# Kernel tuning notes

Hardware: AMD Instinct MI355X
Metric: run time of the kernel (lower is better)

## Reference

```python
import jax, jax.numpy as jnp
from jax import lax
import numpy as np

SEQ, BATCH, IN, HID = 1024, 8192, 3, 50


def setup_inputs() -> dict:
    key = jax.random.key(0)
    ks = jax.random.split(key, 7)
    s_ih = 1.0 / np.sqrt(HID)
    return {
        "x": jax.random.normal(ks[0], (SEQ, BATCH, IN), dtype=jnp.float32),
        "W_ih": jax.random.normal(ks[1], (4 * HID, IN), dtype=jnp.float32) * s_ih,
        "W_hh": jax.random.normal(ks[2], (4 * HID, HID), dtype=jnp.float32) * s_ih,
        "b_ih": jax.random.normal(ks[3], (4 * HID,), dtype=jnp.float32) * s_ih,
        "b_hh": jax.random.normal(ks[4], (4 * HID,), dtype=jnp.float32) * s_ih,
        "fc_w": jax.random.normal(ks[5], (1, HID), dtype=jnp.float32) * s_ih,
        "fc_b": jax.random.normal(ks[6], (1,), dtype=jnp.float32) * s_ih,
    }


def reference(x, W_ih, W_hh, b_ih, b_hh, fc_w, fc_b):
    # x: (T, B, I); PyTorch LSTM gate order is i, f, g, o along the 4H axis.
    T, B, _ = x.shape
    H = W_hh.shape[1]
    # Hoist the input projection out of the recurrence: one big GEMM.
    xg = jnp.einsum("tbi,gi->tbg", x, W_ih) + b_ih + b_hh  # (T, B, 4H)

    def step(carry, xg_t):
        h, c = carry
        gates = xg_t + h @ W_hh.T  # (B, 4H)
        i, f, g, o = jnp.split(gates, 4, axis=-1)
        i = jax.nn.sigmoid(i)
        f = jax.nn.sigmoid(f)
        g = jnp.tanh(g)
        o = jax.nn.sigmoid(o)
        c = f * c + i * g
        h = o * jnp.tanh(c)
        return (h, c), None

    h0 = jnp.zeros((B, H), dtype=x.dtype)
    c0 = jnp.zeros((B, H), dtype=x.dtype)
    (h_last, _), _ = lax.scan(step, (h0, c0), xg)
    # h.squeeze(0) in the torch code -> last layer's final hidden state (B, H)
    return h_last @ fc_w.T + fc_b  # (B, 1)
```

## Files before the change

kernel.cpp:

```cpp
#include <hip/hip_runtime.h>

#define SEQ   1024
#define BATCH 8192
#define HID   50
#define BT    32
#define CHS   16
#define NCH   (SEQ/CHS)
#define CHF   (CHS*BT*3)

typedef _Float16 half8 __attribute__((ext_vector_type(8)));
typedef float    f32x4 __attribute__((ext_vector_type(4)));

__device__ __forceinline__ int bslot(int k, int b){
  return (k >> 5)*512 + ((k & 31) >> 3)*128 + b*8 + (k & 7);
}

#define MFMA16(A,B,C) __builtin_amdgcn_mfma_f32_16x16x32_f16(A,B,C,0,0,0)

#define XLD(cg) {                                                          \
    const int f1 = tid + 512, f2 = tid + 1024;                             \
    const int s0_ = (tid*683) >> 16, s1_ = (f1*683) >> 16,                 \
              s2_ = (f2*683) >> 16;                                        \
    xr0 = x[(size_t)(((cg)*CHS + s0_)*BATCH + b0)*3 + (tid - 96*s0_)];     \
    xr1 = x[(size_t)(((cg)*CHS + s1_)*BATCH + b0)*3 + (f1  - 96*s1_)];     \
    xr2 = x[(size_t)(((cg)*CHS + s2_)*BATCH + b0)*3 + (f2  - 96*s2_)]; }

#define ELEM(acc, C, bq, slot) {                                              \
    const float Ei = __builtin_amdgcn_exp2f((acc)[0]);                        \
    const float Ef = __builtin_amdgcn_exp2f((acc)[1]);                        \
    const float Eg = __builtin_amdgcn_exp2f(fminf((acc)[2], 60.0f));          \
    const float Eo = __builtin_amdgcn_exp2f((acc)[3]);                        \
    const float di = 1.0f + Ei, df = 1.0f + Ef, dg = 1.0f + Eg;               \
    const float digg = di*dg;                                                 \
    const float r1 = __builtin_amdgcn_rcpf(digg*df);                          \
    const float t2 = __builtin_fmaf(Eg, 2.88539008177792f,                    \
                                    -2.88539008177792f);                      \
    const float num = __builtin_fmaf(C, digg, t2*df);                         \
    C = num*r1;                                                               \
    const float Ec = __builtin_amdgcn_exp2f(fminf(C, 80.0f));                 \
    const float r2 = __builtin_amdgcn_rcpf((1.0f+Eo)*(1.0f+Ec));              \
    (bq)[slot] = (_Float16)((Ec - 1.0f)*r2); }

__global__ __launch_bounds__(512, 2)
void lstm_g3(const float* __restrict__ x,
             const float* __restrict__ W_ih,
             const float* __restrict__ W_hh,
             const float* __restrict__ b_ih,
             const float* __restrict__ b_hh,
             const float* __restrict__ fc_w,
             const float* __restrict__ fc_b,
             float* __restrict__ out)
{
  __shared__ _Float16 Bst[2][2][1024];
  __shared__ float    xb[2][CHF];

  const int tid  = threadIdx.x;
  const int w    = tid >> 6;
  const int lane = tid & 63;
  const int r16  = lane & 15;
  const int grp  = lane >> 4;
  const int b0   = blockIdx.x * BT;
  const float L2E = 1.44269504088896f;

  const int  t1    = w;
  const int  t2    = (w < 5) ? (8 + w) : (5 + w);
  const bool hasA2 = (w < 5);
  const bool hasB2 = (w < 2) || (w >= 5);

  half8 Af[2][2];
  #pragma unroll
  for (int it = 0; it < 2; ++it) {
    const int tile = it ? t2 : t1;
    #pragma unroll
    for (int kh = 0; kh < 2; ++kh) {
      half8 f;
      #pragma unroll
      for (int i = 0; i < 8; ++i) {
        const int k = kh*32 + grp*8 + i;
        const int c = tile*16 + r16;
        float wv = 0.0f;
        if (c < 4*HID) {
          const int j = c >> 2, gi = c & 3;
          const int go = gi*HID + j;
          const float sc = (gi == 2) ? (2.0f*L2E) : (-L2E);
          if (k < HID)      wv = W_hh[go*HID + k] * sc;
          else if (k < 53)  wv = W_ih[go*3 + (k-50)] * sc;
          else if (k == 53) wv = (b_ih[go] + b_hh[go]) * sc;
        }
        f[i] = (_Float16)wv;
      }
      Af[it][kh] = f;
    }
  }

  const int j2  = t2*4 + grp;
  const int ws1 = bslot(t1*4 + grp, r16);
  const int ws2 = bslot((j2 < HID) ? j2 : 0, r16);
  const bool m2 = (j2 < HID);

  #pragma unroll
  for (int i = 0; i < 4; ++i) ((unsigned*)Bst)[tid + 512*i] = 0u;
  __syncthreads();
  if (tid < 64) Bst[tid >> 5][(tid >> 4) & 1][768 + (tid & 15)*8 + 5] = (_Float16)1.0f;

  float xr0, xr1, xr2;
  XLD(0); xb[0][tid] = xr0; xb[0][tid+512] = xr1; xb[0][tid+1024] = xr2;
  XLD(1); xb[1][tid] = xr0; xb[1][tid+512] = xr1; xb[1][tid+1024] = xr2;
  XLD(2);
  __syncthreads();
  if (tid < 96) {
    const int g = tid >= 48, l = tid - 48*g;
    const int bb = (l*171) >> 9, e = l - 3*bb;
    Bst[g][0][768 + bb*8 + 2 + e] = (_Float16)xb[0][tid];
  }
  __syncthreads();

  float csA0 = 0.f, csA1 = 0.f, csB0 = 0.f, csB1 = 0.f;

  auto step = [&](int t, int p, int q) {
    _Float16* bqA = &Bst[0][q][0];
    _Float16* bqB = &Bst[1][q][0];
    if ((w == 6 || w == 7) && lane < 48) {
      const int tn = t + 1;
      const int bb = (lane*171) >> 9, e = lane - 3*bb;
      const float xv = xb[(tn >> 4) & 1][(tn & 15)*96 + (w - 6)*48 + lane];
      (w == 6 ? bqA : bqB)[768 + bb*8 + 2 + e] = (_Float16)xv;
    }
    const half8 sA0 = *(const half8*)&Bst[0][p][lane*8];
    const half8 sA1 = *(const half8*)&Bst[0][p][512 + lane*8];
    const half8 sB0 = *(const half8*)&Bst[1][p][lane*8];
    const half8 sB1 = *(const half8*)&Bst[1][p][512 + lane*8];
    f32x4 aA0 = {0.f,0.f,0.f,0.f}, aB0 = {0.f,0.f,0.f,0.f};
    aA0 = MFMA16(Af[0][0], sA0, aA0);  aA0 = MFMA16(Af[0][1], sA1, aA0);
    aB0 = MFMA16(Af[0][0], sB0, aB0);  aB0 = MFMA16(Af[0][1], sB1, aB0);
    if (hasA2) {
      f32x4 aA1 = {0.f,0.f,0.f,0.f};
      aA1 = MFMA16(Af[1][0], sA0, aA1);  aA1 = MFMA16(Af[1][1], sA1, aA1);
      if (m2) ELEM(aA1, csA1, bqA, ws2);
    }
    if (hasB2) {
      f32x4 aB1 = {0.f,0.f,0.f,0.f};
      aB1 = MFMA16(Af[1][0], sB0, aB1);  aB1 = MFMA16(Af[1][1], sB1, aB1);
      if (m2) ELEM(aB1, csB1, bqB, ws2);
    }
    ELEM(aA0, csA0, bqA, ws1);
    ELEM(aB0, csB0, bqB, ws1);
    asm volatile("s_waitcnt lgkmcnt(0)\n\ts_barrier" ::: "memory");
  };

  #pragma unroll 1
  for (int tc = 0; tc < NCH; ++tc) {
    if (tc > 0) {
      const int pc = (tc + 1) & 1;
      xb[pc][tid] = xr0; xb[pc][tid+512] = xr1; xb[pc][tid+1024] = xr2;
      if (tc + 2 < NCH) { XLD(tc+2); }
    }
    const int tb = tc*CHS;
    #pragma unroll 1
    for (int u = 0; u < CHS/2; ++u) {
      step(tb + 2*u,     0, 1);
      step(tb + 2*u + 1, 1, 0);
    }
  }

  __syncthreads();
  if (tid < BT) {
    const int g = tid >> 4, b = tid & 15;
    float s = fc_b[0];
    #pragma unroll
    for (int j = 0; j < HID; ++j)
      s += fc_w[j] * (float)Bst[g][0][bslot(j, b)];
    out[b0 + tid] = s;
  }
}

extern "C" void kernel_launch(void* const* d_in, const int* in_sizes, int n_in,
                              void* d_out, int out_size, void* d_ws, size_t ws_size,
                              hipStream_t stream)
{
  const float* x    = (const float*)d_in[0];
  const float* W_ih = (const float*)d_in[1];
  const float* W_hh = (const float*)d_in[2];
  const float* b_ih = (const float*)d_in[3];
  const float* b_hh = (const float*)d_in[4];
  const float* fc_w = (const float*)d_in[5];
  const float* fc_b = (const float*)d_in[6];
  lstm_g3<<<BATCH/BT, 512, 65536, stream>>>(x, W_ih, W_hh, b_ih, b_hh,
                                            fc_w, fc_b, (float*)d_out);
}
```

Before: 555.6 us.

## Halve batch tile to 16 per block with 4 waves and inline x injection

```diff
diff --git a/kernel.cpp b/kernel.cpp
--- a/kernel.cpp
+++ b/kernel.cpp
@@ -3,10 +3,9 @@
 #define SEQ   1024
 #define BATCH 8192
 #define HID   50
-#define BT    32
+#define BT    16
 #define CHS   16
 #define NCH   (SEQ/CHS)
-#define CHF   (CHS*BT*3)
 
 typedef _Float16 half8 __attribute__((ext_vector_type(8)));
 typedef float    f32x4 __attribute__((ext_vector_type(4)));
@@ -18,12 +17,23 @@
 #define MFMA16(A,B,C) __builtin_amdgcn_mfma_f32_16x16x32_f16(A,B,C,0,0,0)
 
 #define XLD(cg) {                                                          \
-    const int f1 = tid + 512, f2 = tid + 1024;                             \
-    const int s0_ = (tid*683) >> 16, s1_ = (f1*683) >> 16,                 \
-              s2_ = (f2*683) >> 16;                                        \
-    xr0 = x[(size_t)(((cg)*CHS + s0_)*BATCH + b0)*3 + (tid - 96*s0_)];     \
-    xr1 = x[(size_t)(((cg)*CHS + s1_)*BATCH + b0)*3 + (f1  - 96*s1_)];     \
-    xr2 = x[(size_t)(((cg)*CHS + s2_)*BATCH + b0)*3 + (f2  - 96*s2_)]; }
+    const int f1 = tid + 256, f2 = tid + 512;                              \
+    const int s0_ = (tid*683) >> 15, s1_ = (f1*683) >> 15,                 \
+              s2_ = (f2*683) >> 15;                                        \
+    xr0 = x[(size_t)(((cg)*CHS + s0_)*BATCH + b0)*3 + (tid - 48*s0_)];     \
+    xr1 = x[(size_t)(((cg)*CHS + s1_)*BATCH + b0)*3 + (f1  - 48*s1_)];     \
+    xr2 = x[(size_t)(((cg)*CHS + s2_)*BATCH + b0)*3 + (f2  - 48*s2_)]; }
+
+#define XCOMMIT(bf) {                                                      \
+    const int f1 = tid + 256, f2 = tid + 512;                              \
+    const int s0_ = (tid*683) >> 15, s1_ = (f1*683) >> 15,                 \
+              s2_ = (f2*683) >> 15;                                        \
+    const int r0_ = tid - 48*s0_, r1_ = f1 - 48*s1_, r2_ = f2 - 48*s2_;    \
+    const int b0_ = (r0_*171) >> 9, b1_ = (r1_*171) >> 9,                  \
+              b2_ = (r2_*171) >> 9;                                        \
+    xs[bf][s0_][b0_][r0_ - 3*b0_] = (_Float16)xr0;                         \
+    xs[bf][s1_][b1_][r1_ - 3*b1_] = (_Float16)xr1;                         \
+    xs[bf][s2_][b2_][r2_ - 3*b2_] = (_Float16)xr2; }
 
 #define ELEM(acc, C, bq, slot) {                                              \
     const float Ei = __builtin_amdgcn_exp2f((acc)[0]);                        \
@@ -41,8 +51,8 @@
     const float r2 = __builtin_amdgcn_rcpf((1.0f+Eo)*(1.0f+Ec));              \
     (bq)[slot] = (_Float16)((Ec - 1.0f)*r2); }
 
-__global__ __launch_bounds__(512, 2)
-void lstm_g3(const float* __restrict__ x,
+__global__ __launch_bounds__(256, 2)
+void lstm_ph(const float* __restrict__ x,
              const float* __restrict__ W_ih,
              const float* __restrict__ W_hh,
              const float* __restrict__ b_ih,
@@ -51,8 +61,8 @@
              const float* __restrict__ fc_b,
              float* __restrict__ out)
 {
-  __shared__ _Float16 Bst[2][2][1024];
-  __shared__ float    xb[2][CHF];
+  __shared__ _Float16 Bst[2][1024];
+  __shared__ _Float16 xs[2][CHS][16][4];
 
   const int tid  = threadIdx.x;
   const int w    = tid >> 6;
@@ -62,15 +72,13 @@
   const int b0   = blockIdx.x * BT;
   const float L2E = 1.44269504088896f;
 
-  const int  t1    = w;
-  const int  t2    = (w < 5) ? (8 + w) : (5 + w);
-  const bool hasA2 = (w < 5);
-  const bool hasB2 = (w < 2) || (w >= 5);
+  const int  vw = (blockIdx.x & 1) ? (3 - w) : w;
+  const int  nt = (vw == 3) ? 4 : 3;
 
-  half8 Af[2][2];
+  half8 Af[4][2];
   #pragma unroll
-  for (int it = 0; it < 2; ++it) {
-    const int tile = it ? t2 : t1;
+  for (int it = 0; it < 4; ++it) {
+    const int tile = (it < 3) ? (vw + 4*it) : 12;
     #pragma unroll
     for (int kh = 0; kh < 2; ++kh) {
       half8 f;
@@ -93,83 +101,73 @@
     }
   }
 
-  const int j2  = t2*4 + grp;
-  const int ws1 = bslot(t1*4 + grp, r16);
-  const int ws2 = bslot((j2 < HID) ? j2 : 0, r16);
-  const bool m2 = (j2 < HID);
+  int wsl[4];
+  #pragma unroll
+  for (int it = 0; it < 4; ++it) {
+    const int tile = (it < 3) ? (vw + 4*it) : 12;
+    const int j = tile*4 + grp;
+    wsl[it] = bslot((j < HID) ? j : 0, r16);
+  }
 
   #pragma unroll
-  for (int i = 0; i < 4; ++i) ((unsigned*)Bst)[tid + 512*i] = 0u;
-  __syncthreads();
-  if (tid < 64) Bst[tid >> 5][(tid >> 4) & 1][768 + (tid & 15)*8 + 5] = (_Float16)1.0f;
+  for (int i = 0; i < 4; ++i) ((unsigned*)Bst)[tid + 256*i] = 0u;
+  #pragma unroll
+  for (int i2 = 0; i2 < 2; ++i2) {
+    const int i = tid + 256*i2;
+    xs[i >> 8][(i >> 4) & 15][i & 15][3] = (_Float16)1.0f;
+  }
 
   float xr0, xr1, xr2;
-  XLD(0); xb[0][tid] = xr0; xb[0][tid+512] = xr1; xb[0][tid+1024] = xr2;
-  XLD(1); xb[1][tid] = xr0; xb[1][tid+512] = xr1; xb[1][tid+1024] = xr2;
-  XLD(2);
-  __syncthreads();
-  if (tid < 96) {
-    const int g = tid >= 48, l = tid - 48*g;
-    const int bb = (l*171) >> 9, e = l - 3*bb;
-    Bst[g][0][768 + bb*8 + 2 + e] = (_Float16)xb[0][tid];
-  }
+  XLD(0);
+  XCOMMIT(0);
+  XLD(1);
   __syncthreads();
 
-  float csA0 = 0.f, csA1 = 0.f, csB0 = 0.f, csB1 = 0.f;
+  if (blockIdx.x & 1) __builtin_amdgcn_s_sleep(4);
 
-  auto step = [&](int t, int p, int q) {
-    _Float16* bqA = &Bst[0][q][0];
-    _Float16* bqB = &Bst[1][q][0];
-    if ((w == 6 || w == 7) && lane < 48) {
-      const int tn = t + 1;
-      const int bb = (lane*171) >> 9, e = lane - 3*bb;
-      const float xv = xb[(tn >> 4) & 1][(tn & 15)*96 + (w - 6)*48 + lane];
-      (w == 6 ? bqA : bqB)[768 + bb*8 + 2 + e] = (_Float16)xv;
+  float cs[4] = {0.f, 0.f, 0.f, 0.f};
+  const _Float16* xsp = &xs[0][0][0][0];
+
+  auto STEP = [&](int tsv, int p, int q) {
+    const half8 s0 = *(const half8*)&Bst[p][lane*8];
+    uint4 s1d = *(const uint4*)&Bst[p][512 + lane*8];
+    const uint2 xd = *(const uint2*)&xsp[tsv*64 + r16*4];
+    if (grp == 2) { s1d.y = xd.x; s1d.z = xd.y; }
+    const half8 s1 = __builtin_bit_cast(half8, s1d);
+    f32x4 a[4];
+    #pragma unroll
+    for (int it = 0; it < 4; ++it) if (it < nt) {
+      f32x4 z = {0.f, 0.f, 0.f, 0.f};
+      z = MFMA16(Af[it][0], s0, z);
+      a[it] = MFMA16(Af[it][1], s1, z);
     }
-    const half8 sA0 = *(const half8*)&Bst[0][p][lane*8];
-    const half8 sA1 = *(const half8*)&Bst[0][p][512 + lane*8];
-    const half8 sB0 = *(const half8*)&Bst[1][p][lane*8];
-    const half8 sB1 = *(const half8*)&Bst[1][p][512 + lane*8];
-    f32x4 aA0 = {0.f,0.f,0.f,0.f}, aB0 = {0.f,0.f,0.f,0.f};
-    aA0 = MFMA16(Af[0][0], sA0, aA0);  aA0 = MFMA16(Af[0][1], sA1, aA0);
-    aB0 = MFMA16(Af[0][0], sB0, aB0);  aB0 = MFMA16(Af[0][1], sB1, aB0);
-    if (hasA2) {
-      f32x4 aA1 = {0.f,0.f,0.f,0.f};
-      aA1 = MFMA16(Af[1][0], sA0, aA1);  aA1 = MFMA16(Af[1][1], sA1, aA1);
-      if (m2) ELEM(aA1, csA1, bqA, ws2);
-    }
-    if (hasB2) {
-      f32x4 aB1 = {0.f,0.f,0.f,0.f};
-      aB1 = MFMA16(Af[1][0], sB0, aB1);  aB1 = MFMA16(Af[1][1], sB1, aB1);
-      if (m2) ELEM(aB1, csB1, bqB, ws2);
-    }
-    ELEM(aA0, csA0, bqA, ws1);
-    ELEM(aB0, csB0, bqB, ws1);
+    _Float16* bq = &Bst[q][0];
+    #pragma unroll
+    for (int it = 0; it < 3; ++it) ELEM(a[it], cs[it], bq, wsl[it]);
+    if (nt == 4 && grp < 2) ELEM(a[3], cs[3], bq, wsl[3]);
     asm volatile("s_waitcnt lgkmcnt(0)\n\ts_barrier" ::: "memory");
   };
 
   #pragma unroll 1
   for (int tc = 0; tc < NCH; ++tc) {
-    if (tc > 0) {
-      const int pc = (tc + 1) & 1;
-      xb[pc][tid] = xr0; xb[pc][tid+512] = xr1; xb[pc][tid+1024] = xr2;
+    if (tc + 1 < NCH) {
+      XCOMMIT((tc + 1) & 1);
       if (tc + 2 < NCH) { XLD(tc+2); }
     }
-    const int tb = tc*CHS;
-    #pragma unroll 1
-    for (int u = 0; u < CHS/2; ++u) {
-      step(tb + 2*u,     0, 1);
-      step(tb + 2*u + 1, 1, 0);
+    xsp = &xs[tc & 1][0][0][0];
+    #pragma unroll 2
+    for (int ts = 0; ts < CHS; ts += 2) {
+      STEP(ts,     0, 1);
+      STEP(ts + 1, 1, 0);
     }
   }
 
   __syncthreads();
   if (tid < BT) {
-    const int g = tid >> 4, b = tid & 15;
     float s = fc_b[0];
     #pragma unroll
     for (int j = 0; j < HID; ++j)
-      s += fc_w[j] * (float)Bst[g][0][bslot(j, b)];
+      s += fc_w[j] * (float)Bst[0][bslot(j, tid)];
     out[b0 + tid] = s;
   }
 }
@@ -185,6 +183,6 @@
   const float* b_hh = (const float*)d_in[4];
   const float* fc_w = (const float*)d_in[5];
   const float* fc_b = (const float*)d_in[6];
-  lstm_g3<<<BATCH/BT, 512, 65536, stream>>>(x, W_ih, W_hh, b_ih, b_hh,
-                                            fc_w, fc_b, (float*)d_out);
+  lstm_ph<<<BATCH/BT, 256, 0, stream>>>(x, W_ih, W_hh, b_ih, b_hh,
+                                        fc_w, fc_b, (float*)d_out);
 }
```

New measurement: 577.6 us. 3.9% more time.
